# Kernel tuning notes

Measured on AMD Instinct MI355X. Metric: run time of the kernel, lower is better.

## Reference

```python
import jax, jax.numpy as jnp
import numpy as np

EPS = 1e-7  # tf.keras.backend.epsilon()


def squash(v, axis=-1):
    s = jnp.sum(jnp.square(v), axis=axis, keepdims=True)
    scale = s / (1.0 + s) / jnp.sqrt(s + EPS)
    return scale * v


def setup_inputs() -> dict:
    key = jax.random.key(0)
    k1, k2 = jax.random.split(key)
    B, I, D = 64, 2048, 16   # batch, input_num_capsule, input_dim_capsule
    J, K = 32, 16            # num_capsule, dim_capsule
    inputs = jax.random.normal(k1, (B, I, D), dtype=jnp.float32)
    # glorot_uniform-ish init for W: [in_caps, num_caps, in_dim, dim_caps]
    limit = np.sqrt(6.0 / (D + K)).astype(np.float32)
    W = jax.random.uniform(k2, (I, J, D, K), dtype=jnp.float32, minval=-limit, maxval=limit)
    return {"inputs": inputs, "W": W}


def reference(inputs, W, routings=3):
    # u_hat[b,i,j,:] = inputs[b,i,:] @ W[i,j,:,:]
    u_hat = jnp.einsum('bid,ijdk->bijk', inputs, W)  # [B, I, J, K]
    B, I, J, _ = u_hat.shape
    b = jnp.zeros((B, I, J, 1), dtype=u_hat.dtype)
    outputs = None
    for r in range(routings):
        c = jax.nn.softmax(b, axis=2)                              # [B, I, J, 1]
        outputs = squash(jnp.sum(c * u_hat, axis=1, keepdims=True))  # [B, 1, J, K]
        if r < routings - 1:
            b = b + jnp.sum(u_hat * outputs, axis=-1, keepdims=True)
    return jnp.squeeze(outputs, axis=1)  # [B, J, K]
```

## Files before the change

### kernel.cpp

```cpp
#include <hip/hip_runtime.h>
#include <hip/hip_bf16.h>


#define B_ 64
#define I_ 2048
#define D_ 16
#define J_ 32
#define K_ 16
#define JK 512

typedef __attribute__((ext_vector_type(8))) short short8;
typedef __attribute__((ext_vector_type(4))) float float4v;

__device__ __forceinline__ unsigned short f2bf(float f) {
    union { float f; unsigned int i; } v;
    v.f = f;
    const unsigned int x = v.i;
    return (unsigned short)((x + 0x7fffu + ((x >> 16) & 1u)) >> 16);
}

__device__ __forceinline__ void unpack8(const uint4 r, float* u) {
    union { unsigned int i; float f; } t;
    t.i = r.x << 16;         u[0] = t.f;
    t.i = r.x & 0xffff0000u; u[1] = t.f;
    t.i = r.y << 16;         u[2] = t.f;
    t.i = r.y & 0xffff0000u; u[3] = t.f;
    t.i = r.z << 16;         u[4] = t.f;
    t.i = r.z & 0xffff0000u; u[5] = t.f;
    t.i = r.w << 16;         u[6] = t.f;
    t.i = r.w & 0xffff0000u; u[7] = t.f;
}

template <int CTRL>
__device__ __forceinline__ float dpp_add(float x) {
    union { float f; int i; } a, b;
    a.f = x;
    b.i = __builtin_amdgcn_update_dpp(0, a.i, CTRL, 0xf, 0xf, false);
    return x + b.f;
}

__global__ __launch_bounds__(256)
void caps_produce(const float* __restrict__ x, const float* __restrict__ W,
                  unsigned short* __restrict__ uhat) {
    __shared__ unsigned short wlds[32 * 384];
    __shared__ unsigned short zbuf[8];
    __shared__ unsigned short ctile[4][16 * 136];
    const int i = blockIdx.x;
    const int tid = threadIdx.x;

    if (tid < 8) zbuf[tid] = 0;

    const int lane = tid & 63;
    const int wv = tid >> 6;
    const int quad = lane >> 4;
    const int l15 = lane & 15;
    const int b = wv * 16 + l15;

    union { uint4 u; short8 s; } bfrag;
    {
        const float* xp = x + ((size_t)b * I_ + i) * D_ + (quad & 1) * 8;
        const float4 x0 = reinterpret_cast<const float4*>(xp)[0];
        const float4 x1 = reinterpret_cast<const float4*>(xp)[1];
        bfrag.u.x = ((unsigned int)f2bf(x0.y) << 16) | f2bf(x0.x);
        bfrag.u.y = ((unsigned int)f2bf(x0.w) << 16) | f2bf(x0.z);
        bfrag.u.z = ((unsigned int)f2bf(x1.y) << 16) | f2bf(x1.x);
        bfrag.u.w = ((unsigned int)f2bf(x1.w) << 16) | f2bf(x1.z);
        if (quad >= 2) { bfrag.u.x = 0; bfrag.u.y = 0; bfrag.u.z = 0; bfrag.u.w = 0; }
    }

    {
        const float* wbase = W + (size_t)i * (J_ * D_ * K_);
        const int k = tid & 15;
#pragma unroll
        for (int half = 0; half < 2; ++half) {
            const int j = (tid >> 4) + half * 16;
            const float* p = wbase + j * (D_ * K_) + k;
            float vals[16];
#pragma unroll
            for (int d = 0; d < 16; ++d) vals[d] = p[d * K_];
            unsigned int pk[8];
#pragma unroll
            for (int q = 0; q < 8; ++q)
                pk[q] = ((unsigned int)f2bf(vals[2 * q + 1]) << 16) |
                        f2bf(vals[2 * q]);
            uint4* dst = reinterpret_cast<uint4*>(wlds + j * 384 + k * 24);
            uint4 w0; w0.x = pk[0]; w0.y = pk[1]; w0.z = pk[2]; w0.w = pk[3];
            uint4 w1; w1.x = pk[4]; w1.y = pk[5]; w1.z = pk[6]; w1.w = pk[7];
            dst[0] = w0; dst[1] = w1;
        }
    }
    __syncthreads();

    const unsigned short* aptr =
        (quad >= 2) ? zbuf : (wlds + l15 * 24 + (quad & 1) * 8);
    const int astride = (quad >= 2) ? 0 : 384;
    unsigned short* ct = &ctile[wv][0];

    for (int jg = 0; jg < 4; ++jg) {
#pragma unroll
        for (int jj = 0; jj < 8; ++jj) {
            const int j = jg * 8 + jj;
            union { uint4 u; short8 s; } af;
            af.u = *reinterpret_cast<const uint4*>(aptr + (size_t)j * astride);
            float4v acc = {0.f, 0.f, 0.f, 0.f};
            acc = __builtin_amdgcn_mfma_f32_16x16x32_bf16(af.s, bfrag.s, acc,
                                                          0, 0, 0);
            uint2 pk;
            pk.x = ((unsigned int)f2bf(acc[1]) << 16) | f2bf(acc[0]);
            pk.y = ((unsigned int)f2bf(acc[3]) << 16) | f2bf(acc[2]);
            *reinterpret_cast<uint2*>(ct + l15 * 136 + jj * 16 + quad * 4) = pk;
        }
#pragma unroll
        for (int r = 0; r < 4; ++r) {
            const int bsub = r * 4 + (lane >> 4);
            const int c16 = lane & 15;
            const uint4 val = *reinterpret_cast<const uint4*>(
                ct + bsub * 136 + c16 * 8);
            *reinterpret_cast<uint4*>(
                uhat + ((size_t)(wv * 16 + bsub) * I_ + i) * JK + jg * 128 +
                c16 * 8) = val;
        }
    }
}

__global__ __launch_bounds__(256)
void caps_sum0(const unsigned short* __restrict__ uhat,
               float* __restrict__ spart2) {
    __shared__ float part[4][512];
    const int bq = blockIdx.x;
    const int b = bq >> 5, q = bq & 31;
    const int lane = threadIdx.x & 63;
    const int w = threadIdx.x >> 6;

    const unsigned short* up =
        uhat + ((size_t)b * I_ + q * 64 + w * 16) * JK + lane * 8;

    float acc[8];
#pragma unroll
    for (int k = 0; k < 8; ++k) acc[k] = 0.f;

    for (int ii = 0; ii < 16; ii += 4) {
        uint4 r[4];
#pragma unroll
        for (int s = 0; s < 4; ++s)
            r[s] = *reinterpret_cast<const uint4*>(up + (size_t)(ii + s) * JK);
#pragma unroll
        for (int s = 0; s < 4; ++s) {
            float u[8];
            unpack8(r[s], u);
#pragma unroll
            for (int k = 0; k < 8; ++k) acc[k] += u[k];
        }
    }

    float4 o0, o1;
    o0.x = acc[0]; o0.y = acc[1]; o0.z = acc[2]; o0.w = acc[3];
    o1.x = acc[4]; o1.y = acc[5]; o1.z = acc[6]; o1.w = acc[7];
    reinterpret_cast<float4*>(&part[w][lane * 8])[0] = o0;
    reinterpret_cast<float4*>(&part[w][lane * 8])[1] = o1;
    __syncthreads();

    const int t = threadIdx.x;
#pragma unroll
    for (int e = 0; e < 2; ++e) {
        const int jk = t * 2 + e;
        spart2[(size_t)bq * 512 + jk] =
            part[0][jk] + part[1][jk] + part[2][jk] + part[3][jk];
    }
}

__global__ __launch_bounds__(512)
void caps_squash0(const float* __restrict__ spart2, float* __restrict__ vsum) {
    const int bl = blockIdx.x;
    const int jk = threadIdx.x;
    float s = 0.f;
#pragma unroll
    for (int p = 0; p < 32; ++p)
        s += spart2[(size_t)(bl * 32 + p) * 512 + jk];
    s *= (1.f / 32.f);
    float q = s * s;
    q += __shfl_xor(q, 1, 64);
    q += __shfl_xor(q, 2, 64);
    q += __shfl_xor(q, 4, 64);
    q += __shfl_xor(q, 8, 64);
    const float scale = q / ((1.f + q) * sqrtf(q + 1e-7f));
    vsum[bl * JK + jk] = scale * s;
}

__global__ __launch_bounds__(128)
void caps_route1(const unsigned short* __restrict__ uhat,
                 const float* __restrict__ vsum, float* __restrict__ spart) {
    __shared__ float mrg[32][17];
    const int tid = threadIdx.x;
    const int lane = tid & 63;
    const int wv = tid >> 6;
    const int bl = blockIdx.x >> 6;
    const int chunk = blockIdx.x & 63;
    const int h = lane >> 5;
    const int j = lane & 31;

    float v[16];
    {
        const float4* vp =
            reinterpret_cast<const float4*>(vsum + bl * JK + j * 16);
        const float4 a0 = vp[0], a1 = vp[1], a2 = vp[2], a3 = vp[3];
        v[0] = a0.x; v[1] = a0.y; v[2] = a0.z; v[3] = a0.w;
        v[4] = a1.x; v[5] = a1.y; v[6] = a1.z; v[7] = a1.w;
        v[8] = a2.x; v[9] = a2.y; v[10] = a2.z; v[11] = a2.w;
        v[12] = a3.x; v[13] = a3.y; v[14] = a3.z; v[15] = a3.w;
    }

    float acc[16];
#pragma unroll
    for (int k = 0; k < 16; ++k) acc[k] = 0.f;

    const unsigned short* up =
        uhat + ((size_t)bl * I_ + chunk * 32 + wv * 16 + h) * JK + j * 16;

    uint4 c0 = reinterpret_cast<const uint4*>(up)[0];
    uint4 c1 = reinterpret_cast<const uint4*>(up)[1];

#pragma unroll 4
    for (int t = 0; t < 8; ++t) {
        uint4 n0, n1;
        if (t < 7) {
            const uint4* np =
                reinterpret_cast<const uint4*>(up + (size_t)(t + 1) * 2 * JK);
            n0 = np[0];
            n1 = np[1];
        }
        float u[16];
        unpack8(c0, u);
        unpack8(c1, u + 8);
        float p = 0.f;
#pragma unroll
        for (int k = 0; k < 16; ++k) p += u[k] * v[k];
        const float e = __expf(p);
        float S = e;
        S = dpp_add<0x111>(S);
        S = dpp_add<0x112>(S);
        S = dpp_add<0x114>(S);
        S = dpp_add<0x118>(S);
        S = dpp_add<0x142>(S);
        union { float f; int i; } sv, lo, hi;
        sv.f = S;
        lo.i = __builtin_amdgcn_readlane(sv.i, 31);
        hi.i = __builtin_amdgcn_readlane(sv.i, 63);
        const float Ssel = (h == 0) ? lo.f : hi.f;
        const float c = e * __builtin_amdgcn_rcpf(Ssel);
#pragma unroll
        for (int k = 0; k < 16; ++k) acc[k] += c * u[k];
        c0 = n0;
        c1 = n1;
    }

#pragma unroll
    for (int k = 0; k < 16; ++k) acc[k] += __shfl_xor(acc[k], 32, 64);

    if (wv == 1 && h == 0) {
#pragma unroll
        for (int k = 0; k < 16; ++k) mrg[j][k] = acc[k];
    }
    __syncthreads();

    if (wv == 0 && h == 0) {
        float* sp = spart + ((size_t)chunk * B_ + bl) * JK + j * 16;
#pragma unroll
        for (int q = 0; q < 4; ++q) {
            float4 o;
            o.x = acc[q * 4 + 0] + mrg[j][q * 4 + 0];
            o.y = acc[q * 4 + 1] + mrg[j][q * 4 + 1];
            o.z = acc[q * 4 + 2] + mrg[j][q * 4 + 2];
            o.w = acc[q * 4 + 3] + mrg[j][q * 4 + 3];
            reinterpret_cast<float4*>(sp)[q] = o;
        }
    }
}

template <int MODE>
__global__ __launch_bounds__(512)
void caps_squash(const float* __restrict__ spart, float* __restrict__ vsum,
                 float* __restrict__ out) {
    const int bl = blockIdx.x;
    const int jk = threadIdx.x;
    float s = 0.f;
#pragma unroll 8
    for (int p = 0; p < 64; ++p)
        s += spart[((size_t)p * B_ + bl) * JK + jk];
    float q = s * s;
    q += __shfl_xor(q, 1, 64);
    q += __shfl_xor(q, 2, 64);
    q += __shfl_xor(q, 4, 64);
    q += __shfl_xor(q, 8, 64);
    const float scale = q / ((1.f + q) * sqrtf(q + 1e-7f));
    const float v = scale * s;
    if (MODE == 1) vsum[bl * JK + jk] += v;
    else           out[(size_t)bl * JK + jk] = v;
}

extern "C" void kernel_launch(void* const* d_in, const int* in_sizes, int n_in,
                              void* d_out, int out_size, void* d_ws,
                              size_t ws_size, hipStream_t stream) {
    const float* x = (const float*)d_in[0];
    const float* W = (const float*)d_in[1];
    float* out = (float*)d_out;

    char* ws = (char*)d_ws;
    unsigned short* uhat = (unsigned short*)ws;
    float* spart = (float*)(ws + (size_t)B_ * I_ * JK * 2);
    float* vsum = spart + (size_t)64 * B_ * JK;

    caps_produce<<<I_, 256, 0, stream>>>(x, W, uhat);

    caps_sum0<<<2048, 256, 0, stream>>>(uhat, spart);
    caps_squash0<<<B_, 512, 0, stream>>>(spart, vsum);

    caps_route1<<<4096, 128, 0, stream>>>(uhat, vsum, spart);
    caps_squash<1><<<B_, 512, 0, stream>>>(spart, vsum, out);

    caps_route1<<<4096, 128, 0, stream>>>(uhat, vsum, spart);
    caps_squash<2><<<B_, 512, 0, stream>>>(spart, vsum, out);
}
```

Before: 194.1 us.

## Store uhat in [I,B,JK] layout and write MFMA results directly to global

Changes the uhat intermediate layout from batch-major [B,I,JK] to capsule-major [I,B,JK]. The produce kernel then writes each MFMA result straight to global memory, with no LDS staging tile and no extra LDS round trip. The consumer kernels are updated to the new strides. The direct stores are 8-byte uint2 writes scattered across rows rather than coalesced 16-byte rows. Reads in the sum and routing kernels now stride by B*JK per input capsule, which may hurt locality.

```diff
diff --git a/kernel.cpp b/kernel.cpp
--- a/kernel.cpp
+++ b/kernel.cpp
@@ -44,7 +44,6 @@
                   unsigned short* __restrict__ uhat) {
     __shared__ unsigned short wlds[32 * 384];
     __shared__ unsigned short zbuf[8];
-    __shared__ unsigned short ctile[4][16 * 136];
     const int i = blockIdx.x;
     const int tid = threadIdx.x;
 
@@ -94,32 +93,20 @@
     const unsigned short* aptr =
         (quad >= 2) ? zbuf : (wlds + l15 * 24 + (quad & 1) * 8);
     const int astride = (quad >= 2) ? 0 : 384;
-    unsigned short* ct = &ctile[wv][0];
-
-    for (int jg = 0; jg < 4; ++jg) {
-#pragma unroll
-        for (int jj = 0; jj < 8; ++jj) {
-            const int j = jg * 8 + jj;
-            union { uint4 u; short8 s; } af;
-            af.u = *reinterpret_cast<const uint4*>(aptr + (size_t)j * astride);
-            float4v acc = {0.f, 0.f, 0.f, 0.f};
-            acc = __builtin_amdgcn_mfma_f32_16x16x32_bf16(af.s, bfrag.s, acc,
-                                                          0, 0, 0);
-            uint2 pk;
-            pk.x = ((unsigned int)f2bf(acc[1]) << 16) | f2bf(acc[0]);
-            pk.y = ((unsigned int)f2bf(acc[3]) << 16) | f2bf(acc[2]);
-            *reinterpret_cast<uint2*>(ct + l15 * 136 + jj * 16 + quad * 4) = pk;
-        }
-#pragma unroll
-        for (int r = 0; r < 4; ++r) {
-            const int bsub = r * 4 + (lane >> 4);
-            const int c16 = lane & 15;
-            const uint4 val = *reinterpret_cast<const uint4*>(
-                ct + bsub * 136 + c16 * 8);
-            *reinterpret_cast<uint4*>(
-                uhat + ((size_t)(wv * 16 + bsub) * I_ + i) * JK + jg * 128 +
-                c16 * 8) = val;
-        }
+
+    unsigned short* ub = uhat + ((size_t)i * B_ + b) * JK + quad * 4;
+
+#pragma unroll
+    for (int j = 0; j < 32; ++j) {
+        union { uint4 u; short8 s; } af;
+        af.u = *reinterpret_cast<const uint4*>(aptr + (size_t)j * astride);
+        float4v acc = {0.f, 0.f, 0.f, 0.f};
+        acc = __builtin_amdgcn_mfma_f32_16x16x32_bf16(af.s, bfrag.s, acc,
+                                                      0, 0, 0);
+        uint2 pk;
+        pk.x = ((unsigned int)f2bf(acc[1]) << 16) | f2bf(acc[0]);
+        pk.y = ((unsigned int)f2bf(acc[3]) << 16) | f2bf(acc[2]);
+        *reinterpret_cast<uint2*>(ub + j * 16) = pk;
     }
 }
 
@@ -133,7 +120,8 @@
     const int w = threadIdx.x >> 6;
 
     const unsigned short* up =
-        uhat + ((size_t)b * I_ + q * 64 + w * 16) * JK + lane * 8;
+        uhat + ((size_t)(q * 64 + w * 16) * B_ + b) * JK + lane * 8;
+    const size_t istride = (size_t)B_ * JK;
 
     float acc[8];
 #pragma unroll
@@ -143,7 +131,7 @@
         uint4 r[4];
 #pragma unroll
         for (int s = 0; s < 4; ++s)
-            r[s] = *reinterpret_cast<const uint4*>(up + (size_t)(ii + s) * JK);
+            r[s] = *reinterpret_cast<const uint4*>(up + (size_t)(ii + s) * istride);
 #pragma unroll
         for (int s = 0; s < 4; ++s) {
             float u[8];
@@ -215,7 +203,8 @@
     for (int k = 0; k < 16; ++k) acc[k] = 0.f;
 
     const unsigned short* up =
-        uhat + ((size_t)bl * I_ + chunk * 32 + wv * 16 + h) * JK + j * 16;
+        uhat + ((size_t)(chunk * 32 + wv * 16 + h) * B_ + bl) * JK + j * 16;
+    const size_t istride2 = (size_t)2 * B_ * JK;
 
     uint4 c0 = reinterpret_cast<const uint4*>(up)[0];
     uint4 c1 = reinterpret_cast<const uint4*>(up)[1];
@@ -225,7 +214,7 @@
         uint4 n0, n1;
         if (t < 7) {
             const uint4* np =
-                reinterpret_cast<const uint4*>(up + (size_t)(t + 1) * 2 * JK);
+                reinterpret_cast<const uint4*>(up + (size_t)(t + 1) * istride2);
             n0 = np[0];
             n1 = np[1];
         }
```

After: 209.8 us. 1.08x slower.
